# Kernel optimization log

Hardware: AMD Instinct MI355X
Metric: run time of the kernel (lower is better)

Reference implementation:

```python
import jax, jax.numpy as jnp
import numpy as np

DIM = 1024
HEADS = 16
DHEAD = 64
MAXLEN = 512
B = 8
N = 256   # sequence (x) length
M = 256   # memory (h) length; M + N <= MAXLEN
INNER = HEADS * DHEAD


def setup_inputs() -> dict:
    key = jax.random.key(0)
    ks = jax.random.split(key, 8)
    w = lambda k, shape: jax.random.normal(k, shape, jnp.float32) * 0.02
    return {
        "x": jax.random.normal(ks[0], (B, N, DIM), jnp.float32),
        "h": jax.random.normal(ks[1], (B, M, DIM), jnp.float32),
        "Wqkv": w(ks[2], (DIM, 3 * INNER)),
        "Wkr": w(ks[3], (DIM, INNER)),
        "R": jax.random.normal(ks[4], (2 * MAXLEN, DIM), jnp.float32),
        "u": jax.random.normal(ks[5], (DHEAD,), jnp.float32),
        "v": jax.random.normal(ks[6], (DHEAD,), jnp.float32),
        "Wout": w(ks[7], (INNER, DIM)),
        "max_len": MAXLEN,
    }


def reference(x, h, Wqkv, Wkr, R, u, v, Wout, max_len):
    b, n, dim = x.shape
    m = h.shape[1]
    t = m + n
    scale = DHEAD ** -0.5

    cat = jnp.concatenate([h, x], axis=1)                     # [b, t, dim]
    qkv = cat @ Wqkv                                          # [b, t, 3*inner]
    q, k, val = [s.reshape(b, t, HEADS, DHEAD).transpose(0, 2, 1, 3)
                 for s in jnp.split(qkv, 3, axis=-1)]          # [b, h, t, d]

    # shifts[i, j] = (j - i) mod 2L, sliced as in the torch buffer
    ar = jnp.arange(2 * max_len)
    shifts_full = (ar[None, :] - ar[:, None]) % (2 * max_len)
    shifts = shifts_full[:max_len, :max_len][m:m + n, :t]      # [n, t]

    kr = (R @ Wkr)[shifts]                                    # gather: [n, t, inner]
    kr = kr.reshape(n, t, HEADS, DHEAD).transpose(2, 0, 1, 3)  # [h, n, t, d]

    q = q[:, :, m:]                                           # [b, h, n, d]

    term_a = jnp.einsum('bhnd,bhmd->bhnm', q, k)
    term_b = jnp.einsum('bhnd,hnmd->bhnm', q, kr)
    term_c = jnp.einsum('d,bhmd->bhm', u, k)[:, :, None, :]    # broadcast over n
    term_d = jnp.einsum('d,hnmd->hnm', v, kr)[None]            # broadcast over b
    dots = (term_a + term_b + term_c + term_d) * scale         # [b, h, n, t]

    qi = jnp.arange(n)[:, None]
    jm = jnp.arange(m)[None, :]
    js = jnp.arange(n)[None, :]
    mem_mask = jnp.where(qi > jm, -jnp.inf, 0.0)               # [n, m]
    ar_mask = jnp.where(js > qi, -jnp.inf, 0.0)                # [n, n]
    bias = jnp.concatenate([mem_mask, ar_mask], axis=1)[None, None]  # [1,1,n,t]

    attn = jax.nn.softmax(dots + bias, axis=-1)
    out = jnp.einsum('bhnm,bhmd->bhnd', attn, val)             # [b, h, n, d]
    out = out.transpose(0, 2, 1, 3).reshape(b, n, INNER)
    return out @ Wout
```

## Files before the change

### kernel.cpp

```cpp
#include <hip/hip_runtime.h>
#include <hip/hip_bf16.h>
#include <math.h>

typedef unsigned short u16;
typedef short bf16x8 __attribute__((ext_vector_type(8)));
typedef float f32x4 __attribute__((ext_vector_type(4)));

__device__ __forceinline__ u16 f2b(float f) {
    __hip_bfloat16 h = __float2bfloat16(f);
    return *reinterpret_cast<u16*>(&h);
}
__device__ __forceinline__ float b2f(u16 v) {
    __hip_bfloat16 h;
    *reinterpret_cast<u16*>(&h) = v;
    return __bfloat162float(h);
}

__device__ __forceinline__ void gload_lds16(const void* g, void* l) {
    __builtin_amdgcn_global_load_lds(
        (const __attribute__((address_space(1))) void*)g,
        (__attribute__((address_space(3))) void*)l, 16, 0, 0);
}


struct EpiQKV4 {
    u16 *Q, *Kt, *Vt;
    __device__ void operator()(int rowp, int colp, f32x4 vals) const {
        int b = colp >> 9, pos = colp & 511;
        int sec = rowp >> 10, cc = rowp & 1023;
        int head = cc >> 6, d0 = cc & 63;
        ushort4 o;
        if (sec == 0) {
            if (pos < 256) return;
            o.x = f2b(vals[0] * 0.125f); o.y = f2b(vals[1] * 0.125f);
            o.z = f2b(vals[2] * 0.125f); o.w = f2b(vals[3] * 0.125f);
            *(ushort4*)(Q + (long)((head * 8 + b) * 256 + (pos - 256)) * 64 + d0) = o;
        } else {
            u16* dst = (sec == 1) ? Kt : Vt;
            o.x = f2b(vals[0]); o.y = f2b(vals[1]);
            o.z = f2b(vals[2]); o.w = f2b(vals[3]);
            *(ushort4*)(dst + (long)((b * 16 + head) * 512 + pos) * 64 + d0) = o;
        }
    }
};

struct EpiStoreBf {
    u16* C; long ldc; long strideZ;
    __device__ void operator()(int z, int row, int col, float val) const {
        C[(long)z * strideZ + (long)row * ldc + col] = f2b(val);
    }
};

struct EpiStoreF32 {
    float* C; long ldc;
    __device__ void operator()(int z, int row, int col, float val) const {
        C[(long)row * ldc + col] = val;
    }
};


template <typename Epi, bool AF32, bool ADDA, bool ROWMAP>
__device__ __forceinline__ void gemm_bt_body(char* smem, int bx, int by, int bz,
                                             const void* __restrict__ Av, int lda, long strideAz,
                                             const u16* __restrict__ B, int ldb, long strideBz,
                                             int K, Epi epi, const float* __restrict__ av) {
    constexpr int LDT = 56;
    u16* As = (u16*)smem;
    u16* Bs = As + 64 * LDT;
    int n0 = bx * 64, m0 = by * 64, z = bz;
    const u16* Bb = B + (long)z * strideBz + (long)n0 * ldb;
    int tid = threadIdx.x;
    int wave = tid >> 6, lane = tid & 63;
    int wm = wave >> 1, wn = wave & 1;
    int lrow = lane & 15, lquad = lane >> 4;
    int srow = tid >> 2, scol = (tid & 3) * 8;
    f32x4 acc[2][2] = {};
    for (int k0 = 0; k0 < K; k0 += 32) {
        if constexpr (AF32) {
            long arow = m0 + srow;
            if constexpr (ROWMAP) arow = (arow < 256) ? 768 + arow : 0;
            const float* src = (const float*)Av + (long)z * strideAz + arow * lda + k0 + scol;
            float4 f0 = *(const float4*)src;
            float4 f1 = *(const float4*)(src + 4);
            bf16x8 vv;
            vv[0] = (short)f2b(f0.x); vv[1] = (short)f2b(f0.y);
            vv[2] = (short)f2b(f0.z); vv[3] = (short)f2b(f0.w);
            vv[4] = (short)f2b(f1.x); vv[5] = (short)f2b(f1.y);
            vv[6] = (short)f2b(f1.z); vv[7] = (short)f2b(f1.w);
            *(bf16x8*)(As + srow * LDT + scol) = vv;
        } else {
            const u16* Ab = (const u16*)Av + (long)z * strideAz + (long)m0 * lda;
            *(bf16x8*)(As + srow * LDT + scol) = *(const bf16x8*)(Ab + (long)srow * lda + k0 + scol);
        }
        *(bf16x8*)(Bs + srow * LDT + scol) = *(const bf16x8*)(Bb + (long)srow * ldb + k0 + scol);
        __syncthreads();
        bf16x8 af[2], bfr[2];
        #pragma unroll
        for (int mt = 0; mt < 2; ++mt) {
            af[mt] = *(const bf16x8*)(As + (wm * 32 + mt * 16 + lrow) * LDT + lquad * 8);
            if constexpr (ADDA) {
                #pragma unroll
                for (int j = 0; j < 8; ++j)
                    af[mt][j] = (short)f2b(b2f((u16)af[mt][j]) + 0.125f * av[k0 + lquad * 8 + j]);
            }
        }
        #pragma unroll
        for (int nt = 0; nt < 2; ++nt)
            bfr[nt] = *(const bf16x8*)(Bs + (wn * 32 + nt * 16 + lrow) * LDT + lquad * 8);
        #pragma unroll
        for (int mt = 0; mt < 2; ++mt)
            #pragma unroll
            for (int nt = 0; nt < 2; ++nt)
                acc[mt][nt] = __builtin_amdgcn_mfma_f32_16x16x32_bf16(af[mt], bfr[nt], acc[mt][nt], 0, 0, 0);
        __syncthreads();
    }
    #pragma unroll
    for (int mt = 0; mt < 2; ++mt)
        #pragma unroll
        for (int nt = 0; nt < 2; ++nt)
            #pragma unroll
            for (int r = 0; r < 4; ++r) {
                int row = m0 + wm * 32 + mt * 16 + lquad * 4 + r;
                int col = n0 + wn * 32 + nt * 16 + lrow;
                epi(z, row, col, acc[mt][nt][r]);
            }
}

__global__ __launch_bounds__(256) void prep_kernel(const float* __restrict__ x,
                                                   const float* __restrict__ h,
                                                   u16* __restrict__ catBF,
                                                   const float* __restrict__ Wqkv, u16* __restrict__ WqkvT,
                                                   const float* __restrict__ Wkr,  u16* __restrict__ WkrT,
                                                   const float* __restrict__ Wout, u16* __restrict__ WoutT) {
    __shared__ float tile[32][33];
    int bid = blockIdx.x, tid = threadIdx.x;
    if (bid < 2048) {
        int idx = (bid * 256 + tid) * 8;
        int c = idx & 1023, r = idx >> 10;
        int b = r >> 9, pos = r & 511;
        const float* src = (pos < 256) ? h + ((long)(b * 256 + pos) * 1024 + c)
                                       : x + ((long)(b * 256 + pos - 256) * 1024 + c);
        float4 f0 = *(const float4*)src;
        float4 f1 = *(const float4*)(src + 4);
        bf16x8 vv;
        vv[0] = (short)f2b(f0.x); vv[1] = (short)f2b(f0.y);
        vv[2] = (short)f2b(f0.z); vv[3] = (short)f2b(f0.w);
        vv[4] = (short)f2b(f1.x); vv[5] = (short)f2b(f1.y);
        vv[6] = (short)f2b(f1.z); vv[7] = (short)f2b(f1.w);
        *(bf16x8*)(catBF + idx) = vv;
        return;
    }
    const float* W; u16* WT; int nb, kb;
    if (bid < 5120) {
        int w = bid - 2048;
        W = Wqkv; WT = WqkvT;
        nb = (w % 96) * 32; kb = (w / 96) * 32;
        int tx = tid & 31, ty = tid >> 5;
        #pragma unroll
        for (int i = 0; i < 32; i += 8)
            tile[ty + i][tx] = W[(long)(kb + ty + i) * 3072 + nb + tx];
    } else {
        int w = bid - 5120;
        if (w < 1024) { W = Wkr; WT = WkrT; }
        else          { W = Wout; WT = WoutT; w -= 1024; }
        nb = (w & 31) * 32; kb = (w >> 5) * 32;
        int tx = tid & 31, ty = tid >> 5;
        #pragma unroll
        for (int i = 0; i < 32; i += 8)
            tile[ty + i][tx] = W[(long)(kb + ty + i) * 1024 + nb + tx];
    }
    __syncthreads();
    int row = tid >> 3;
    int c4 = (tid & 7) * 4;
    ushort4 o;
    o.x = f2b(tile[c4 + 0][row]);
    o.y = f2b(tile[c4 + 1][row]);
    o.z = f2b(tile[c4 + 2][row]);
    o.w = f2b(tile[c4 + 3][row]);
    *(ushort4*)(WT + (long)(nb + row) * 1024 + kb + c4) = o;
}

__global__ __launch_bounds__(256, 4) void qkv_rwg_kernel(const u16* __restrict__ A, const u16* __restrict__ B,
                                                         EpiQKV4 eq,
                                                         const float* __restrict__ R, const u16* __restrict__ WkrT,
                                                         u16* __restrict__ RWg) {
    __shared__ alignas(16) char smem[32768];
    int bid0 = blockIdx.x;
    if (bid0 >= 640) {
        int bid2 = bid0 - 640;
        gemm_bt_body<EpiStoreBf, true, false, true>(smem, bid2 & 15, bid2 >> 4, 0,
            (const void*)R, 1024, 0L, WkrT, 1024, 0L, 1024, EpiStoreBf{RWg, 1024, 0}, nullptr);
        return;
    }
    int xcd = bid0 & 7, s = bid0 >> 3;
    int G = xcd * 10 + (s >> 3);
    int w = s & 7;
    int m0, n0;
    if (G < 64) {
        int nchunk = G >> 4, mrow = G & 15;
        m0 = 1024 + mrow * 128;
        n0 = (nchunk * 8 + w) * 128;
    } else {
        int G2 = G - 64;
        int nchunk = G2 >> 3, mrow = G2 & 7;
        m0 = mrow * 128;
        int c = nchunk * 8 + w;
        n0 = (c >> 1) * 512 + 256 + (c & 1) * 128;
    }
    int tid = threadIdx.x, wave = tid >> 6, lane = tid & 63;
    int wm = wave >> 1, wn = wave & 1;
    int lrow = lane & 15, lquad = lane >> 4;
    const u16* Ab = A + (long)m0 * 1024;
    const u16* Bb = B + (long)n0 * 1024;
    f32x4 acc[4][4] = {};

    auto stage = [&](int buf, int k0) {
        u16* Asb = (u16*)smem + buf * 8192;
        u16* Bsb = Asb + 4096;
        #pragma unroll
        for (int i = 0; i < 2; ++i) {
            int rowb = i * 64 + (tid >> 2);
            int col = k0 + (tid & 3) * 8;
            gload_lds16(Ab + (long)rowb * 1024 + col, Asb + i * 2048 + tid * 8);
            gload_lds16(Bb + (long)rowb * 1024 + col, Bsb + i * 2048 + tid * 8);
        }
    };
    auto compute = [&](int buf) {
        u16* Asb = (u16*)smem + buf * 8192;
        u16* Bsb = Asb + 4096;
        bf16x8 af[4], bfr[4];
        #pragma unroll
        for (int mt = 0; mt < 4; ++mt)
            af[mt] = *(const bf16x8*)(Asb + (wm * 64 + mt * 16 + lrow) * 32 + lquad * 8);
        #pragma unroll
        for (int nt = 0; nt < 4; ++nt)
            bfr[nt] = *(const bf16x8*)(Bsb + (wn * 64 + nt * 16 + lrow) * 32 + lquad * 8);
        #pragma unroll
        for (int mt = 0; mt < 4; ++mt)
            #pragma unroll
            for (int nt = 0; nt < 4; ++nt)
                acc[mt][nt] = __builtin_amdgcn_mfma_f32_16x16x32_bf16(af[mt], bfr[nt], acc[mt][nt], 0, 0, 0);
    };

    stage(0, 0);
    stage(1, 32);
    for (int t = 0; t < 31; ++t) {
        asm volatile("s_waitcnt vmcnt(4)" ::: "memory");
        __builtin_amdgcn_sched_barrier(0);
        __builtin_amdgcn_s_barrier();
        __builtin_amdgcn_sched_barrier(0);
        compute(t & 1);
        __builtin_amdgcn_sched_barrier(0);
        __builtin_amdgcn_s_barrier();
        __builtin_amdgcn_sched_barrier(0);
        if (t < 30) stage(t & 1, (t + 2) * 32);
    }
    asm volatile("s_waitcnt vmcnt(0)" ::: "memory");
    __builtin_amdgcn_sched_barrier(0);
    __builtin_amdgcn_s_barrier();
    __builtin_amdgcn_sched_barrier(0);
    compute(1);

    #pragma unroll
    for (int mt = 0; mt < 4; ++mt)
        #pragma unroll
        for (int nt = 0; nt < 4; ++nt) {
            int rowp = m0 + wm * 64 + mt * 16 + lquad * 4;
            int colp = n0 + wn * 64 + nt * 16 + lrow;
            eq(rowp, colp, acc[mt][nt]);
        }
}

__global__ __launch_bounds__(256) void vtrans_qr_kernel(const u16* __restrict__ Vtmp, u16* __restrict__ VT,
                                                        const u16* __restrict__ Q, const u16* __restrict__ RWg,
                                                        u16* __restrict__ QR, const float* __restrict__ v) {
    __shared__ alignas(16) char smem[14336];
    int bid = blockIdx.x, tid = threadIdx.x;
    if (bid < 4096) {
        u16 (*tile)[34] = (u16(*)[34])smem;
        int t0 = (bid & 15) * 32, d0 = ((bid >> 4) & 1) * 32, bh = bid >> 5;
        int tx = tid & 31, ty = tid >> 5;
        const u16* src = Vtmp + (long)bh * 512 * 64;
        #pragma unroll
        for (int i = 0; i < 32; i += 8)
            tile[ty + i][tx] = src[(long)(t0 + ty + i) * 64 + d0 + tx];
        __syncthreads();
        u16* dst = VT + (long)bh * 64 * 512;
        #pragma unroll
        for (int i = 0; i < 32; i += 8)
            dst[(long)(d0 + ty + i) * 512 + t0 + tx] = tile[tx][ty + i];
        return;
    }
    int bid2 = bid - 4096;
    int bx = bid2 % 5;
    int rest = bid2 / 5;
    int by = rest & 31, bz = rest >> 5;
    gemm_bt_body<EpiStoreBf, false, true, false>(smem, bx, by, bz,
        (const void*)Q, 64, 2048L * 64, RWg, 1024, 64L, 64,
        EpiStoreBf{QR, 320, 2048L * 320}, v);
}

__global__ __launch_bounds__(256) void outproj_kernel(const u16* __restrict__ A,
                                                      const u16* __restrict__ B,
                                                      float* __restrict__ out) {
    __shared__ alignas(16) char smem[14336];
    gemm_bt_body<EpiStoreF32, false, false, false>(smem, blockIdx.x, blockIdx.y, 0,
        (const void*)A, 1024, 0L, B, 1024, 0L, 1024, EpiStoreF32{out, 1024}, nullptr);
}

__global__ __launch_bounds__(256, 4) void attn_kernel(const u16* __restrict__ Qs,
                                                      const u16* __restrict__ Kt,
                                                      const u16* __restrict__ VT,
                                                      const u16* __restrict__ QR,
                                                      const float* __restrict__ uvec,
                                                      u16* __restrict__ attnOut) {
    constexpr int LDSW = 328;
    __shared__ alignas(16) u16 SQ[32 * LDSW];
    __shared__ float red[2][4][32];
    int id = blockIdx.x;
    int bh = id & 127, it = id >> 7;
    int b = bh >> 4, h = bh & 15;
    int i0 = it * 32;
    int w0 = i0;
    int tid = threadIdx.x, wave = tid >> 6, lane = tid & 63;
    int lrow = lane & 15, lquad = lane >> 4;

    const u16* qrg = QR + ((long)h * 2048 + b * 256 + i0) * 320;
    #pragma unroll
    for (int kk = 0; kk < 5; ++kk) {
        int idx = tid + kk * 256;
        int row = idx / 40, c = idx - row * 40;
        *(bf16x8*)(SQ + row * LDSW + c * 8) = *(const bf16x8*)(qrg + row * 320 + c * 8);
    }

    bf16x8 aq[2][2];
    #pragma unroll
    for (int iu = 0; iu < 2; ++iu) {
        const u16* qbase = Qs + (long)((h * 8 + b) * 256 + i0 + iu * 16 + lrow) * 64;
        aq[iu][0] = *(const bf16x8*)(qbase + lquad * 8);
        aq[iu][1] = *(const bf16x8*)(qbase + 32 + lquad * 8);
        #pragma unroll
        for (int j = 0; j < 8; ++j) {
            aq[iu][0][j] = (short)f2b(b2f((u16)aq[iu][0][j]) + 0.125f * uvec[lquad * 8 + j]);
            aq[iu][1][j] = (short)f2b(b2f((u16)aq[iu][1][j]) + 0.125f * uvec[32 + lquad * 8 + j]);
        }
    }

    const u16* kbase = Kt + ((long)bh * 512 + w0 + wave * 80) * 64;
    bf16x8 bk0[5], bk1[5];
    #pragma unroll
    for (int t = 0; t < 5; ++t) {
        const u16* kp = kbase + (long)(t * 16 + lrow) * 64;
        bk0[t] = *(const bf16x8*)(kp + lquad * 8);
        bk1[t] = *(const bf16x8*)(kp + 32 + lquad * 8);
    }
    f32x4 acc[2][5];
    #pragma unroll
    for (int t = 0; t < 5; ++t)
        #pragma unroll
        for (int iu = 0; iu < 2; ++iu) {
            f32x4 a = {0.f, 0.f, 0.f, 0.f};
            a = __builtin_amdgcn_mfma_f32_16x16x32_bf16(aq[iu][0], bk0[t], a, 0, 0, 0);
            a = __builtin_amdgcn_mfma_f32_16x16x32_bf16(aq[iu][1], bk1[t], a, 0, 0, 0);
            acc[iu][t] = a;
        }
    __syncthreads();

    float m4[2][4];
    #pragma unroll
    for (int iu = 0; iu < 2; ++iu)
        #pragma unroll
        for (int r = 0; r < 4; ++r) m4[iu][r] = -1e30f;
    #pragma unroll
    for (int t = 0; t < 5; ++t) {
        int lj = wave * 80 + t * 16 + lrow;
        #pragma unroll
        for (int iu = 0; iu < 2; ++iu)
            #pragma unroll
            for (int r = 0; r < 4; ++r) {
                int rloc = iu * 16 + lquad * 4 + r;
                int d = lj - rloc;
                int dc = d < 0 ? 0 : (d > 256 ? 256 : d);
                bool ok = (unsigned)d <= 256u;
                float val = ok ? acc[iu][t][r] + b2f(SQ[rloc * LDSW + dc]) : -1e30f;
                acc[iu][t][r] = val;
                m4[iu][r] = fmaxf(m4[iu][r], val);
            }
    }
    #pragma unroll
    for (int iu = 0; iu < 2; ++iu)
        #pragma unroll
        for (int r = 0; r < 4; ++r) {
            #pragma unroll
            for (int off = 1; off < 16; off <<= 1)
                m4[iu][r] = fmaxf(m4[iu][r], __shfl_xor(m4[iu][r], off));
            if (lrow == 0) red[0][wave][iu * 16 + lquad * 4 + r] = m4[iu][r];
        }
    __syncthreads();

    float gmax[2][4];
    #pragma unroll
    for (int iu = 0; iu < 2; ++iu)
        #pragma unroll
        for (int r = 0; r < 4; ++r) {
            int row = iu * 16 + lquad * 4 + r;
            gmax[iu][r] = fmaxf(fmaxf(red[0][0][row], red[0][1][row]),
                                fmaxf(red[0][2][row], red[0][3][row]));
        }

    float s4[2][4] = {};
    #pragma unroll
    for (int t = 0; t < 5; ++t) {
        int lj = wave * 80 + t * 16 + lrow;
        #pragma unroll
        for (int iu = 0; iu < 2; ++iu)
            #pragma unroll
            for (int r = 0; r < 4; ++r) {
                float p = __expf(acc[iu][t][r] - gmax[iu][r]);
                s4[iu][r] += p;
                SQ[(iu * 16 + lquad * 4 + r) * LDSW + lj] = f2b(p);
            }
    }
    #pragma unroll
    for (int iu = 0; iu < 2; ++iu)
        #pragma unroll
        for (int r = 0; r < 4; ++r) {
            #pragma unroll
            for (int off = 1; off < 16; off <<= 1)
                s4[iu][r] += __shfl_xor(s4[iu][r], off);
            if (lrow == 0) red[1][wave][iu * 16 + lquad * 4 + r] = s4[iu][r];
        }
    __syncthreads();

    const u16* vbase = VT + ((long)bh * 64 + wave * 16 + lrow) * 512 + w0;
    f32x4 oacc[2] = {};
    bf16x8 vp[10];
    #pragma unroll
    for (int t = 0; t < 10; ++t)
        vp[t] = *(const bf16x8*)(vbase + t * 32 + lquad * 8);
    #pragma unroll
    for (int t = 0; t < 10; ++t)
        #pragma unroll
        for (int iu = 0; iu < 2; ++iu) {
            bf16x8 ap = *(const bf16x8*)(SQ + (iu * 16 + lrow) * LDSW + t * 32 + lquad * 8);
            oacc[iu] = __builtin_amdgcn_mfma_f32_16x16x32_bf16(ap, vp[t], oacc[iu], 0, 0, 0);
        }
    #pragma unroll
    for (int iu = 0; iu < 2; ++iu)
        #pragma unroll
        for (int r = 0; r < 4; ++r) {
            int row = iu * 16 + lquad * 4 + r;
            float inv = 1.0f / (red[1][0][row] + red[1][1][row] + red[1][2][row] + red[1][3][row]);
            attnOut[(long)(b * 256 + i0 + row) * 1024 + h * 64 + wave * 16 + lrow] = f2b(oacc[iu][r] * inv);
        }
}


extern "C" void kernel_launch(void* const* d_in, const int* in_sizes, int n_in,
                              void* d_out, int out_size, void* d_ws, size_t ws_size,
                              hipStream_t stream) {
    (void)in_sizes; (void)n_in; (void)out_size; (void)ws_size;
    const float* x    = (const float*)d_in[0];
    const float* h    = (const float*)d_in[1];
    const float* Wqkv = (const float*)d_in[2];
    const float* Wkr  = (const float*)d_in[3];
    const float* R    = (const float*)d_in[4];
    const float* u    = (const float*)d_in[5];
    const float* v    = (const float*)d_in[6];
    const float* Wout = (const float*)d_in[7];
    float* out = (float*)d_out;

    char* ws = (char*)d_ws;
    size_t off = 0;
    auto alloc = [&](size_t bytes) -> void* {
        void* p = ws + off;
        off = (off + bytes + 255) & ~(size_t)255;
        return p;
    };
    u16* catBF  = (u16*)alloc(4096L * 1024 * 2);
    u16* WqkvT  = (u16*)alloc(3072L * 1024 * 2);
    u16* WkrT   = (u16*)alloc(1024L * 1024 * 2);
    u16* WoutT  = (u16*)alloc(1024L * 1024 * 2);
    u16* RWg    = (u16*)alloc(320L * 1024 * 2);
    u16* Q      = (u16*)alloc(16L * 8 * 256 * 64 * 2);
    u16* Kt     = (u16*)alloc(8L * 16 * 512 * 64 * 2);
    u16* Vtmp   = (u16*)alloc(8L * 16 * 512 * 64 * 2);
    u16* VT     = (u16*)alloc(8L * 16 * 64 * 512 * 2);
    u16* QR     = (u16*)alloc(16L * 2048 * 320 * 2);
    u16* attnO  = (u16*)alloc(2048L * 1024 * 2);

    prep_kernel<<<7168, 256, 0, stream>>>(x, h, catBF, Wqkv, WqkvT, Wkr, WkrT, Wout, WoutT);
    qkv_rwg_kernel<<<720, 256, 0, stream>>>(WqkvT, catBF, EpiQKV4{Q, Kt, Vtmp}, R, WkrT, RWg);
    vtrans_qr_kernel<<<6656, 256, 0, stream>>>(Vtmp, VT, Q, RWg, QR, v);
    attn_kernel<<<1024, 256, 0, stream>>>(Q, Kt, VT, QR, u, attnO);
    outproj_kernel<<<dim3(16, 32), 256, 0, stream>>>(attnO, WoutT, out);
}
```

Baseline: 177.5 us.

## Fuse V transpose into QKV epilogue and compute Q·R bias inside attention

The QKV GEMM epilogue now writes V directly in transposed (d-major) layout, which removes the separate V-transpose pass. The Q·(R Wkr) relative-position term is computed inside the attention kernel with MFMA from RWg and staged in LDS, which removes the QR intermediate buffer and the vtrans_qr kernel launch. In exchange, the transposed V stores are scalar and strided, so they are less coalesced, and each attention block does extra MFMA work and RWg loads. A guard region is zeroed past VT.

```diff
diff --git a/kernel.cpp b/kernel.cpp
--- a/kernel.cpp
+++ b/kernel.cpp
@@ -29,17 +29,21 @@
         int b = colp >> 9, pos = colp & 511;
         int sec = rowp >> 10, cc = rowp & 1023;
         int head = cc >> 6, d0 = cc & 63;
-        ushort4 o;
         if (sec == 0) {
             if (pos < 256) return;
+            ushort4 o;
             o.x = f2b(vals[0] * 0.125f); o.y = f2b(vals[1] * 0.125f);
             o.z = f2b(vals[2] * 0.125f); o.w = f2b(vals[3] * 0.125f);
             *(ushort4*)(Q + (long)((head * 8 + b) * 256 + (pos - 256)) * 64 + d0) = o;
-        } else {
-            u16* dst = (sec == 1) ? Kt : Vt;
+        } else if (sec == 1) {
+            ushort4 o;
             o.x = f2b(vals[0]); o.y = f2b(vals[1]);
             o.z = f2b(vals[2]); o.w = f2b(vals[3]);
-            *(ushort4*)(dst + (long)((b * 16 + head) * 512 + pos) * 64 + d0) = o;
+            *(ushort4*)(Kt + (long)((b * 16 + head) * 512 + pos) * 64 + d0) = o;
+        } else {
+            #pragma unroll
+            for (int r = 0; r < 4; ++r)
+                Vt[(long)((b * 16 + head) * 64 + d0 + r) * 512 + pos] = f2b(vals[r]);
         }
     }
 };
@@ -131,9 +135,14 @@
                                                    u16* __restrict__ catBF,
                                                    const float* __restrict__ Wqkv, u16* __restrict__ WqkvT,
                                                    const float* __restrict__ Wkr,  u16* __restrict__ WkrT,
-                                                   const float* __restrict__ Wout, u16* __restrict__ WoutT) {
+                                                   const float* __restrict__ Wout, u16* __restrict__ WoutT,
+                                                   u16* __restrict__ vtGuard) {
     __shared__ float tile[32][33];
     int bid = blockIdx.x, tid = threadIdx.x;
+    if (bid == 7168) {
+        ((unsigned int*)vtGuard)[tid] = 0u;
+        return;
+    }
     if (bid < 2048) {
         int idx = (bid * 256 + tid) * 8;
         int c = idx & 1023, r = idx >> 10;
@@ -271,35 +280,6 @@
         }
 }
 
-__global__ __launch_bounds__(256) void vtrans_qr_kernel(const u16* __restrict__ Vtmp, u16* __restrict__ VT,
-                                                        const u16* __restrict__ Q, const u16* __restrict__ RWg,
-                                                        u16* __restrict__ QR, const float* __restrict__ v) {
-    __shared__ alignas(16) char smem[14336];
-    int bid = blockIdx.x, tid = threadIdx.x;
-    if (bid < 4096) {
-        u16 (*tile)[34] = (u16(*)[34])smem;
-        int t0 = (bid & 15) * 32, d0 = ((bid >> 4) & 1) * 32, bh = bid >> 5;
-        int tx = tid & 31, ty = tid >> 5;
-        const u16* src = Vtmp + (long)bh * 512 * 64;
-        #pragma unroll
-        for (int i = 0; i < 32; i += 8)
-            tile[ty + i][tx] = src[(long)(t0 + ty + i) * 64 + d0 + tx];
-        __syncthreads();
-        u16* dst = VT + (long)bh * 64 * 512;
-        #pragma unroll
-        for (int i = 0; i < 32; i += 8)
-            dst[(long)(d0 + ty + i) * 512 + t0 + tx] = tile[tx][ty + i];
-        return;
-    }
-    int bid2 = bid - 4096;
-    int bx = bid2 % 5;
-    int rest = bid2 / 5;
-    int by = rest & 31, bz = rest >> 5;
-    gemm_bt_body<EpiStoreBf, false, true, false>(smem, bx, by, bz,
-        (const void*)Q, 64, 2048L * 64, RWg, 1024, 64L, 64,
-        EpiStoreBf{QR, 320, 2048L * 320}, v);
-}
-
 __global__ __launch_bounds__(256) void outproj_kernel(const u16* __restrict__ A,
                                                       const u16* __restrict__ B,
                                                       float* __restrict__ out) {
@@ -311,8 +291,9 @@
 __global__ __launch_bounds__(256, 4) void attn_kernel(const u16* __restrict__ Qs,
                                                       const u16* __restrict__ Kt,
                                                       const u16* __restrict__ VT,
-                                                      const u16* __restrict__ QR,
+                                                      const u16* __restrict__ RWg,
                                                       const float* __restrict__ uvec,
+                                                      const float* __restrict__ vvec,
                                                       u16* __restrict__ attnOut) {
     constexpr int LDSW = 328;
     __shared__ alignas(16) u16 SQ[32 * LDSW];
@@ -325,24 +306,37 @@
     int tid = threadIdx.x, wave = tid >> 6, lane = tid & 63;
     int lrow = lane & 15, lquad = lane >> 4;
 
-    const u16* qrg = QR + ((long)h * 2048 + b * 256 + i0) * 320;
-    #pragma unroll
-    for (int kk = 0; kk < 5; ++kk) {
-        int idx = tid + kk * 256;
-        int row = idx / 40, c = idx - row * 40;
-        *(bf16x8*)(SQ + row * LDSW + c * 8) = *(const bf16x8*)(qrg + row * 320 + c * 8);
-    }
-
-    bf16x8 aq[2][2];
+    bf16x8 aq[2][2], aqv[2][2];
     #pragma unroll
     for (int iu = 0; iu < 2; ++iu) {
         const u16* qbase = Qs + (long)((h * 8 + b) * 256 + i0 + iu * 16 + lrow) * 64;
-        aq[iu][0] = *(const bf16x8*)(qbase + lquad * 8);
-        aq[iu][1] = *(const bf16x8*)(qbase + 32 + lquad * 8);
+        bf16x8 q0 = *(const bf16x8*)(qbase + lquad * 8);
+        bf16x8 q1 = *(const bf16x8*)(qbase + 32 + lquad * 8);
         #pragma unroll
         for (int j = 0; j < 8; ++j) {
-            aq[iu][0][j] = (short)f2b(b2f((u16)aq[iu][0][j]) + 0.125f * uvec[lquad * 8 + j]);
-            aq[iu][1][j] = (short)f2b(b2f((u16)aq[iu][1][j]) + 0.125f * uvec[32 + lquad * 8 + j]);
+            float f0 = b2f((u16)q0[j]), f1 = b2f((u16)q1[j]);
+            aq[iu][0][j]  = (short)f2b(f0 + 0.125f * uvec[lquad * 8 + j]);
+            aq[iu][1][j]  = (short)f2b(f1 + 0.125f * uvec[32 + lquad * 8 + j]);
+            aqv[iu][0][j] = (short)f2b(f0 + 0.125f * vvec[lquad * 8 + j]);
+            aqv[iu][1][j] = (short)f2b(f1 + 0.125f * vvec[32 + lquad * 8 + j]);
+        }
+    }
+
+    const u16* rwbase = RWg + (long)(wave * 80) * 1024 + h * 64;
+    #pragma unroll
+    for (int t = 0; t < 5; ++t) {
+        const u16* rp = rwbase + (long)(t * 16 + lrow) * 1024;
+        bf16x8 br0 = *(const bf16x8*)(rp + lquad * 8);
+        bf16x8 br1 = *(const bf16x8*)(rp + 32 + lquad * 8);
+        int sc = wave * 80 + t * 16 + lrow;
+        #pragma unroll
+        for (int iu = 0; iu < 2; ++iu) {
+            f32x4 qa = {0.f, 0.f, 0.f, 0.f};
+            qa = __builtin_amdgcn_mfma_f32_16x16x32_bf16(aqv[iu][0], br0, qa, 0, 0, 0);
+            qa = __builtin_amdgcn_mfma_f32_16x16x32_bf16(aqv[iu][1], br1, qa, 0, 0, 0);
+            #pragma unroll
+            for (int r = 0; r < 4; ++r)
+                SQ[(iu * 16 + lquad * 4 + r) * LDSW + sc] = f2b(qa[r]);
         }
     }
 
@@ -484,14 +478,12 @@
     u16* RWg    = (u16*)alloc(320L * 1024 * 2);
     u16* Q      = (u16*)alloc(16L * 8 * 256 * 64 * 2);
     u16* Kt     = (u16*)alloc(8L * 16 * 512 * 64 * 2);
-    u16* Vtmp   = (u16*)alloc(8L * 16 * 512 * 64 * 2);
-    u16* VT     = (u16*)alloc(8L * 16 * 64 * 512 * 2);
-    u16* QR     = (u16*)alloc(16L * 2048 * 320 * 2);
+    u16* VT     = (u16*)alloc(8L * 16 * 64 * 512 * 2 + 1024);
     u16* attnO  = (u16*)alloc(2048L * 1024 * 2);
-
-    prep_kernel<<<7168, 256, 0, stream>>>(x, h, catBF, Wqkv, WqkvT, Wkr, WkrT, Wout, WoutT);
-    qkv_rwg_kernel<<<720, 256, 0, stream>>>(WqkvT, catBF, EpiQKV4{Q, Kt, Vtmp}, R, WkrT, RWg);
-    vtrans_qr_kernel<<<6656, 256, 0, stream>>>(Vtmp, VT, Q, RWg, QR, v);
-    attn_kernel<<<1024, 256, 0, stream>>>(Q, Kt, VT, QR, u, attnO);
+    u16* vtGuard = VT + 8L * 16 * 64 * 512;
+
+    prep_kernel<<<7169, 256, 0, stream>>>(x, h, catBF, Wqkv, WqkvT, Wkr, WkrT, Wout, WoutT, vtGuard);
+    qkv_rwg_kernel<<<720, 256, 0, stream>>>(WqkvT, catBF, EpiQKV4{Q, Kt, VT}, R, WkrT, RWg);
+    attn_kernel<<<1024, 256, 0, stream>>>(Q, Kt, VT, RWg, u, v, attnO);
     outproj_kernel<<<dim3(16, 32), 256, 0, stream>>>(attnO, WoutT, out);
 }
```

Result: faster. 166.8 us (-6.0%).
